# Kernel tuning notes

Hardware: AMD Instinct MI355X
Metric: run time of the kernel (lower is better)

Reference implementation:

```python
import jax, jax.numpy as jnp
import numpy as np

D = 256       # vec_dim
HEADS = 8     # head_num
PS = 4        # patch_size
WS = 7        # window_size (in patches)
P = WS * WS   # tokens per window


def _relative_index():
    # replicates the torch meshgrid / relative coord logic (indexing='ij')
    coords = np.stack(np.meshgrid(np.arange(WS), np.arange(WS), indexing='ij'))  # [2,WS,WS]
    cf = coords.reshape(2, -1)                                                   # [2,P]
    rc = (cf[:, :, None] - cf[:, None, :]).transpose(1, 2, 0)                    # [P,P,2]
    rc[:, :, 0] += WS - 1
    rc[:, :, 1] += WS - 1
    rc[:, :, 1] *= 2 * WS - 1
    return rc.sum(-1)  # [P,P] ints in [0,(2WS-1)^2)


def _shift_mask(ch, cw):
    # standard swin shift mask built on the patch grid (ch, cw)
    fm = np.zeros((ch, cw))
    idx = (slice(0, -WS), slice(-WS, -(WS // 2)), slice(-(WS // 2), None))
    cnt = 0
    for y in idx:
        for x in idx:
            fm[y, x] = cnt
            cnt += 1
    nh, nw = ch // WS, cw // WS
    fm = fm.reshape(nh, WS, nw, WS).transpose(0, 2, 1, 3).reshape(nh * nw, P)
    m = fm[:, None, :] - fm[:, :, None]
    return np.where(m != 0, -100.0, 0.0).astype(np.float32)


def setup_inputs() -> dict:
    key = jax.random.key(0)
    ks = jax.random.split(key, 10)
    N, PN = 8, 3136
    s = 0.02
    return {
        'inputs': jax.random.normal(ks[0], (N, D, PN), jnp.float32),
        'Wk': jax.random.normal(ks[1], (HEADS * D, D), jnp.float32) * s,
        'bk': jax.random.normal(ks[2], (HEADS * D,), jnp.float32) * s,
        'Wq': jax.random.normal(ks[3], (HEADS * D, D), jnp.float32) * s,
        'bq': jax.random.normal(ks[4], (HEADS * D,), jnp.float32) * s,
        'Wv': jax.random.normal(ks[5], (HEADS * D, D), jnp.float32) * s,
        'bv': jax.random.normal(ks[6], (HEADS * D,), jnp.float32) * s,
        'Wo': jax.random.normal(ks[7], (D, HEADS * D), jnp.float32) * s,
        'bo': jax.random.normal(ks[8], (D,), jnp.float32) * s,
        'rel_code': jax.random.normal(ks[9], ((2 * WS - 1) ** 2, HEADS), jnp.float32) * 0.02,
        'h': 224,
        'w': 224,
    }


def _forward(inputs, Wk, bk, Wq, bq, Wv, bv, Wo, bo, rel_code, h, w):
    ch, cw = h // PS, w // PS            # patch grid
    N, _, PN = inputs.shape
    C = D // (PS * PS)
    nh, nw = ch // WS, cw // WS
    WIN = nh * nw

    # patches2features -> pixel-space roll by WS//2 -> features2patches
    x = inputs.reshape(N, C, PS, PS, ch, cw)
    x = x.transpose(0, 1, 4, 2, 5, 3).reshape(N, C, ch * PS, cw * PS)
    x = jnp.roll(x, (WS // 2, WS // 2), axis=(-2, -1))
    x = x.reshape(N, C, ch, PS, cw, PS).transpose(0, 2, 4, 1, 3, 5).reshape(N, PN, D)
    x = x.transpose(0, 2, 1)  # [N,D,PN]

    def proj(W, b):
        e = jnp.einsum('od,ndp->nop', W, x) + b[None, :, None]  # [N,HEADS*D,PN]
        e = e.reshape(N, HEADS, D, ch, cw)
        # window partition: n h d (nh w1)(nw w2) -> n h (nh nw) d (w1 w2)
        e = e.reshape(N, HEADS, D, nh, WS, nw, WS)
        return e.transpose(0, 1, 3, 5, 2, 4, 6).reshape(N, HEADS, WIN, D, P)

    k = proj(Wk, bk)
    q = proj(Wq, bq)
    v = proj(Wv, bv)

    # attn[p,q] = k_p . q_q  (softmax over keys p, axis=3)
    attn = jnp.einsum('nhgdp,nhgdq->nhgpq', k, q) / (D ** 0.5)
    mask = jnp.asarray(_shift_mask(ch, cw))
    attn = attn + mask[None, None]
    rel_idx = _relative_index().ravel()
    rel = rel_code[rel_idx].reshape(P, P, HEADS).transpose(2, 0, 1)  # [H,P,P]
    attn = attn + rel[None, :, None]
    wmap = jax.nn.softmax(attn, axis=3)

    out = jnp.einsum('nhgdp,nhgpq->nhgdq', v, wmap)
    # window merge back to [N,H,D,PN]
    out = out.reshape(N, HEADS, nh, nw, D, WS, WS)
    out = out.transpose(0, 1, 4, 2, 5, 3, 6).reshape(N, HEADS * D, PN)
    return jnp.einsum('od,ndp->nop', Wo, out) + bo[None, :, None]  # [N,D,PN]


def reference(inputs, Wk, bk, Wq, bq, Wv, bv, Wo, bo, rel_code, h, w):
    return _forward(inputs, Wk, bk, Wq, bq, Wv, bv, Wo, bo, rel_code, h, w)
```

## Files before the change

### kernel.cpp

```cpp
#include <hip/hip_runtime.h>
#include <hip/hip_bf16.h>


#define NBATCH 8
#define MSTR   2176
#define TROWS  3200

typedef unsigned short ushort_t;
typedef __attribute__((ext_vector_type(8))) short bf16x8;
typedef __attribute__((ext_vector_type(8))) unsigned short u16x8;
typedef __attribute__((ext_vector_type(4))) float f32x4;

__device__ __forceinline__ float b2f(ushort_t u) {
  union { unsigned int i; float f; } v; v.i = ((unsigned int)u) << 16; return v.f;
}
__device__ __forceinline__ ushort_t f2b(float f) {
  union { float f; unsigned int u; } v; v.f = f;
  unsigned int u = v.u;
  return (ushort_t)((u + 0x7FFFu + ((u >> 16) & 1u)) >> 16);
}
__device__ __forceinline__ int regof(int y) { return (y < 49) ? 0 : ((y < 53) ? 1 : 2); }
__device__ __forceinline__ int div7(int t) { return (t * 37) >> 8; }
__device__ __forceinline__ int tmap(int p, int gi, int gj) {
  int wi = div7(p); return (gi * 7 + wi) * 56 + gj * 7 + (p - wi * 7);
}
__device__ __forceinline__ ushort4 pack4(f32x4 a) {
  ushort4 u; u.x = f2b(a[0]); u.y = f2b(a[1]); u.z = f2b(a[2]); u.w = f2b(a[3]);
  return u;
}
__device__ __forceinline__ void gload_lds16(const ushort_t* g, ushort_t* l) {
  __builtin_amdgcn_global_load_lds(
      (const __attribute__((address_space(1))) void*)g,
      (__attribute__((address_space(3))) void*)l, 16, 0, 0);
}
__device__ __forceinline__ void sb0() { __builtin_amdgcn_sched_barrier(0); }

__global__ void k_prep(const float* __restrict__ Wk, const float* __restrict__ Wq,
                       const float* __restrict__ Wo, const float* __restrict__ Wv,
                       const float* __restrict__ bk, const float* __restrict__ bq,
                       const float* __restrict__ bv, const float* __restrict__ bo,
                       const float* __restrict__ relc,
                       ushort_t* __restrict__ Aext, ushort_t* __restrict__ Wov3,
                       float* __restrict__ cvec, float* __restrict__ relL2) {
  __shared__ float red[8];
  int blk = blockIdx.x, t = threadIdx.x;
  if (blk < 512) {
    int h = blk >> 6, b0 = (blk & 63) << 2, a = t;
    const float* wkh = Wk + h * 65536;
    const float* wqh = Wq + h * 65536;
    float a0 = 0.f, a1 = 0.f, a2 = 0.f, a3 = 0.f;
    for (int dd = 0; dd < 256; ++dd) {
      float wk = wkh[dd * 256 + a];
      float4 w4 = *(const float4*)(wqh + dd * 256 + b0);
      a0 += wk * w4.x; a1 += wk * w4.y; a2 += wk * w4.z; a3 += wk * w4.w;
    }
    ushort4 u; u.x = f2b(a0); u.y = f2b(a1); u.z = f2b(a2); u.w = f2b(a3);
    *(ushort4*)(Aext + (h * 256 + a) * 256 + b0) = u;
  } else if (blk < 1024) {
    int bb = blk - 512;
    int h = bb >> 6, o0 = (bb & 63) << 2, d = t;
    float a0 = 0.f, a1 = 0.f, a2 = 0.f, a3 = 0.f;
    for (int dd = 0; dd < 256; ++dd) {
      float wv = Wv[(h * 256 + dd) * 256 + d];
      a0 += Wo[(o0 + 0) * 2048 + h * 256 + dd] * wv;
      a1 += Wo[(o0 + 1) * 2048 + h * 256 + dd] * wv;
      a2 += Wo[(o0 + 2) * 2048 + h * 256 + dd] * wv;
      a3 += Wo[(o0 + 3) * 2048 + h * 256 + dd] * wv;
    }
    Wov3[(o0 + 0) * 2048 + h * 256 + d] = f2b(a0);
    Wov3[(o0 + 1) * 2048 + h * 256 + d] = f2b(a1);
    Wov3[(o0 + 2) * 2048 + h * 256 + d] = f2b(a2);
    Wov3[(o0 + 3) * 2048 + h * 256 + d] = f2b(a3);
  } else if (blk < 1032) {
    int h = blk - 1024;
    float s1 = 0.f, s2 = 0.f;
    for (int dd = 0; dd < 256; ++dd) {
      s1 += bk[h * 256 + dd] * Wq[(h * 256 + dd) * 256 + t];
      s2 += bq[h * 256 + dd] * Wk[(h * 256 + dd) * 256 + t];
    }
    Aext[(2048 + h) * 256 + t] = f2b(s1);
    Aext[(2056 + h) * 256 + t] = f2b(s2);
  } else if (blk == 1032) {
    for (int i = t; i < 112 * 256 / 8; i += 256)
      *(u16x8*)(Aext + 2064 * 256 + i * 8) = (u16x8){0,0,0,0,0,0,0,0};
  } else if (blk < 1289) {
    int o = blk - 1033;
    const float* wob = Wo + o * 2048;
    float acc = 0.f;
#pragma unroll
    for (int j = 0; j < 8; ++j) acc += wob[j * 256 + t] * bv[j * 256 + t];
#pragma unroll
    for (int s = 1; s < 64; s <<= 1) acc += __shfl_xor(acc, s);
    if ((t & 63) == 0) red[t >> 6] = acc;
    __syncthreads();
    if (t == 0) cvec[o] = bo[o] + red[0] + red[1] + red[2] + red[3];
  } else {
    if (t < 8) {
      float c = 0.f;
      for (int dd = 0; dd < 256; ++dd) c += bk[t * 256 + dd] * bq[t * 256 + dd];
      red[t] = c * 0.0625f;
    }
    __syncthreads();
    for (int i = t; i < 8 * 169; i += 256) {
      int h = i / 169, idx = i - h * 169;
      relL2[i] = relc[idx * 8 + h] + red[h];
    }
  }
}

__global__ void k_conv(const float* __restrict__ X, ushort_t* __restrict__ Xroll) {
  const int n = blockIdx.x / 57, y = blockIdx.x % 57;
  ushort_t* xr = Xroll + (size_t)n * TROWS * 256;
  const int d = threadIdx.x;
  if (y == 56) {
    for (int i = d; i < 64 * 256 / 8; i += 256)
      *(u16x8*)(xr + 3136 * 256 + i * 8) = (u16x8){0,0,0,0,0,0,0,0};
    return;
  }
  const int c = d >> 4, p1 = (d >> 2) & 3, p2 = d & 3;
  const int sp = c * 16 + (((p1 + 1) & 3) << 2) + ((p2 + 1) & 3);
  const int ty = (p1 == 3) ? y : ((y == 0) ? 55 : y - 1);
  const float* rowp = X + (size_t)n * 256 * 3136 + sp * 3136 + ty * 56;
  ushort_t* orow = xr + y * 56 * 256 + d;
  for (int x = 0; x < 56; ++x) {
    int tx = (p2 == 3) ? x : ((x == 0) ? 55 : x - 1);
    orow[x * 256] = f2b(rowp[tx]);
  }
}

__global__ __launch_bounds__(256, 2) void k_gemm1(
    const ushort_t* __restrict__ Xroll, const ushort_t* __restrict__ Aext,
    ushort_t* __restrict__ MT) {
  __shared__ ushort_t Bsm[2][64 * 256];
  const int bx0 = blockIdx.x;
  const int n = bx0 & 7;
  const int inner = bx0 >> 3;
  const int aa = inner % 17;
  const int c  = inner / 17;
  const int a0 = aa * 128;
  const int tstart = (c == 0) ? 0 : (7 * c + 1);
  const int T = (c == 0) ? 8 : 7;
  const int tid = threadIdx.x, wave = tid >> 6, lane = tid & 63;
  const int quad = lane >> 4, l16 = lane & 15;
  const int wa = wave >> 1, wt = wave & 1;
  const ushort_t* Xn = Xroll + (size_t)n * TROWS * 256;
  ushort_t* Mn = MT + (size_t)n * TROWS * MSTR;

  const ushort_t* abase = Aext + (size_t)(a0 + wa * 64 + l16) * 256 + quad * 8;
  bf16x8 areg[8][4];
#pragma unroll
  for (int kk = 0; kk < 8; ++kk)
#pragma unroll
    for (int i = 0; i < 4; ++i)
      areg[kk][i] = *(const bf16x8*)(abase + i * 4096 + kk * 32);
  sb0();

  auto fill = [&](int mt, int b) {
    const ushort_t* src = Xn + (size_t)(tstart + mt) * 64 * 256;
#pragma unroll
    for (int i = 0; i < 8; ++i) {
      int S = i * 256 + tid;
      int rr = S >> 5, sc = S & 31;
      int cc = (sc & 24) | ((sc ^ rr) & 7);
      gload_lds16(src + rr * 256 + cc * 8, &Bsm[b][(i * 256 + wave * 64) * 8]);
    }
  };

  fill(0, 0); sb0();
  fill(1, 1); sb0();
  asm volatile("s_waitcnt vmcnt(8)" ::: "memory"); sb0();
  __builtin_amdgcn_s_barrier(); sb0();

  const int sw = l16 & 7;
  for (int m = 0; m < T; ++m) {
    if (m > 0) {
      if (m + 1 < T) { asm volatile("s_waitcnt vmcnt(16)" ::: "memory"); }
      else           { asm volatile("s_waitcnt vmcnt(8)"  ::: "memory"); }
      sb0();
      __builtin_amdgcn_s_barrier(); sb0();
    }
    const int b = m & 1;
    f32x4 acc[4][2];
#pragma unroll
    for (int i = 0; i < 4; ++i)
#pragma unroll
      for (int j = 0; j < 2; ++j) acc[i][j] = (f32x4){0.f, 0.f, 0.f, 0.f};
#pragma unroll
    for (int kk = 0; kk < 8; ++kk) {
      bf16x8 bfj[2];
#pragma unroll
      for (int j = 0; j < 2; ++j) {
        int rr = wt * 32 + j * 16 + l16;
        int cc = kk * 4 + quad;
        int pos = (cc & 24) | ((cc ^ sw) & 7);
        bfj[j] = *(const bf16x8*)(&Bsm[b][rr * 256 + pos * 8]);
      }
#pragma unroll
      for (int i = 0; i < 4; ++i)
#pragma unroll
        for (int j = 0; j < 2; ++j)
          acc[i][j] = __builtin_amdgcn_mfma_f32_16x16x32_bf16(areg[kk][i], bfj[j], acc[i][j], 0, 0, 0);
    }
    const int tb = (tstart + m) * 64;
#pragma unroll
    for (int i = 0; i < 4; ++i)
#pragma unroll
      for (int j = 0; j < 2; ++j) {
        int tg = tb + wt * 32 + j * 16 + l16;
        int ag = a0 + wa * 64 + i * 16 + quad * 4;
        *(ushort4*)(Mn + (size_t)tg * MSTR + ag) = pack4(acc[i][j]);
      }
    sb0();
    __builtin_amdgcn_s_barrier(); sb0();
    if (m + 2 < T) { fill(m + 2, b); sb0(); }
  }
}

#define XP_STR 264
__global__ __launch_bounds__(512, 4) void k_attn2(
    const ushort_t* __restrict__ Xroll, ushort_t* __restrict__ MT,
    const float* __restrict__ relL2) {
  __shared__ ushort_t Xp[64 * XP_STR];
  __shared__ ushort_t StB[2][64 * 72];
  __shared__ float aqsL[8 * 64];
  __shared__ float bpsL[8 * 64];
  __shared__ float relLh[8 * 169];

  const int tid = threadIdx.x;
  const int wave = tid >> 6, lane = tid & 63;
  const int quad = lane >> 4, l16 = lane & 15;
  const int group = wave >> 2, wv = wave & 3;
  const int n = blockIdx.x >> 6, g = blockIdx.x & 63;
  const int gi = g >> 3, gj = g & 7;
  const ushort_t* Xn = Xroll + (size_t)n * TROWS * 256;
  ushort_t* Mn = MT + (size_t)n * TROWS * MSTR;

  {
    const int p = tid & 63, cg = tid >> 6;
    if (p < 49) {
      int t = tmap(p, gi, gj);
#pragma unroll
      for (int i = 0; i < 4; ++i)
        *(u16x8*)(&Xp[p * XP_STR + (cg * 4 + i) * 8]) =
            *(const u16x8*)(Xn + t * 256 + (cg * 4 + i) * 8);
    } else {
#pragma unroll
      for (int i = 0; i < 4; ++i)
        *(u16x8*)(&Xp[p * XP_STR + (cg * 4 + i) * 8]) = (u16x8){0,0,0,0,0,0,0,0};
    }
  }
  for (int i = tid; i < 8 * 169; i += 512) relLh[i] = relL2[i];
  {
    const int h = tid >> 6, q = tid & 63;
    int qq = (q < 49) ? q : 48;
    int t = tmap(qq, gi, gj);
    aqsL[h * 64 + q] = b2f(Mn[(size_t)t * MSTR + 2048 + h]);
    bpsL[h * 64 + q] = b2f(Mn[(size_t)t * MSTR + 2056 + h]);
  }
  __syncthreads();

  bf16x8 xfr[4][2];
#pragma unroll
  for (int dt = 0; dt < 4; ++dt) {
    const int d = (wv * 4 + dt) * 16 + l16;
#pragma unroll
    for (int kk = 0; kk < 2; ++kk)
#pragma unroll
      for (int j = 0; j < 8; ++j)
        xfr[dt][kk][j] = (short)Xp[(kk * 32 + quad * 8 + j) * XP_STR + d];
  }

  const int q = wv * 16 + l16;
  const int qq = (q < 49) ? q : 48;
  const int tq = tmap(qq, gi, gj);
  const ushort_t* Mbase = Mn + (size_t)tq * MSTR + quad * 8;
  const int yq = div7(qq), xq = qq - yq * 7;
  const int fq = regof(gi * 7 + yq) * 3 + regof(gj * 7 + xq);

  for (int hh = 0; hh < 4; ++hh) {
    const int h = hh * 2 + group;
    f32x4 sacc[4];
#pragma unroll
    for (int pt = 0; pt < 4; ++pt) sacc[pt] = (f32x4){0.f, 0.f, 0.f, 0.f};
    const ushort_t* mrow = Mbase + h * 256;
#pragma unroll
    for (int kk = 0; kk < 8; ++kk) {
      bf16x8 bfm = *(const bf16x8*)(mrow + kk * 32);
#pragma unroll
      for (int pt = 0; pt < 4; ++pt) {
        bf16x8 af = *(const bf16x8*)(&Xp[(pt * 16 + l16) * XP_STR + kk * 32 + quad * 8]);
        sacc[pt] = __builtin_amdgcn_mfma_f32_16x16x32_bf16(af, bfm, sacc[pt], 0, 0, 0);
      }
    }
    float v[16];
    const float aqv = aqsL[h * 64 + q];
    const float* rel_h = &relLh[h * 169];
    float m = -1e30f;
#pragma unroll
    for (int pt = 0; pt < 4; ++pt)
#pragma unroll
      for (int r = 0; r < 4; ++r) {
        int p = pt * 16 + quad * 4 + r;
        float val = -1e30f;
        if (p < 49) {
          int yp = div7(p), xp = p - yp * 7;
          int fp = regof(gi * 7 + yp) * 3 + regof(gj * 7 + xp);
          val = (sacc[pt][r] + aqv + bpsL[h * 64 + p]) * 0.0625f +
                rel_h[(yp - yq + 6) + 13 * (xp - xq + 6)];
          if (fp != fq) val -= 100.f;
        }
        v[pt * 4 + r] = val;
        m = fmaxf(m, val);
      }
    m = fmaxf(m, __shfl_xor(m, 16));
    m = fmaxf(m, __shfl_xor(m, 32));
    float s = 0.f;
#pragma unroll
    for (int i = 0; i < 16; ++i) { v[i] = __expf(v[i] - m); s += v[i]; }
    s += __shfl_xor(s, 16);
    s += __shfl_xor(s, 32);
    const float inv = 1.f / s;
    __syncthreads();
    {
      ushort_t* sb = &StB[group][q * 72];
#pragma unroll
      for (int pt = 0; pt < 4; ++pt) {
        ushort4 u;
        u.x = f2b(v[pt * 4 + 0] * inv); u.y = f2b(v[pt * 4 + 1] * inv);
        u.z = f2b(v[pt * 4 + 2] * inv); u.w = f2b(v[pt * 4 + 3] * inv);
        *(ushort4*)(&sb[pt * 16 + quad * 4]) = u;
      }
    }
    __syncthreads();
#pragma unroll
    for (int qt = 0; qt < 4; ++qt) {
      f32x4 tacc[4];
#pragma unroll
      for (int dt = 0; dt < 4; ++dt) tacc[dt] = (f32x4){0.f, 0.f, 0.f, 0.f};
#pragma unroll
      for (int kk = 0; kk < 2; ++kk) {
        bf16x8 bfw = *(const bf16x8*)(&StB[group][(qt * 16 + l16) * 72 + kk * 32 + quad * 8]);
#pragma unroll
        for (int dt = 0; dt < 4; ++dt)
          tacc[dt] = __builtin_amdgcn_mfma_f32_16x16x32_bf16(xfr[dt][kk], bfw, tacc[dt], 0, 0, 0);
      }
      int q2 = qt * 16 + l16;
      if (q2 < 49) {
        int t2 = tmap(q2, gi, gj);
#pragma unroll
        for (int dt = 0; dt < 4; ++dt) {
          int d0 = (wv * 4 + dt) * 16 + quad * 4;
          *(ushort4*)(Mn + (size_t)t2 * MSTR + h * 256 + d0) = pack4(tacc[dt]);
        }
      }
    }
  }
}

__global__ __launch_bounds__(256, 2) void k_gemm3(
    const ushort_t* __restrict__ Wov3, const ushort_t* __restrict__ MT,
    const float* __restrict__ cvec, float* __restrict__ out) {
  __shared__ ushort_t Asm[128 * 128];
  __shared__ ushort_t Bsm[128 * 128];
  const int bx0 = blockIdx.x;
  const int bx = (bx0 & 7) * 50 + (bx0 >> 3);
  const int n = bx / 50, r2 = bx % 50;
  const int oi = r2 / 25, tt = r2 % 25;
  const int o0 = oi * 128, t0 = tt * 128;
  const int tid = threadIdx.x, wave = tid >> 6, lane = tid & 63;
  const int quad = lane >> 4, l16 = lane & 15;
  const int wa = wave >> 1, wt = wave & 1;
  const ushort_t* Tn = MT + (size_t)n * TROWS * MSTR;
  float* on = out + (size_t)n * 256 * 3136;
  const int sw = l16 & 7;

  f32x4 acc[4][4];
#pragma unroll
  for (int i = 0; i < 4; ++i)
#pragma unroll
    for (int j = 0; j < 4; ++j) acc[i][j] = (f32x4){0.f, 0.f, 0.f, 0.f};

  for (int kit = 0; kit < 16; ++kit) {
    const int kb = kit * 128;
#pragma unroll
    for (int i = 0; i < 8; ++i) {
      int S = i * 256 + tid;
      int rr = S >> 4, sc = S & 15;
      int c = (sc & 8) | ((sc ^ rr) & 7);
      gload_lds16(Wov3 + (o0 + rr) * 2048 + kb + c * 8,
                  &Asm[(i * 256 + wave * 64) * 8]);
    }
#pragma unroll
    for (int i = 0; i < 8; ++i) {
      int S = i * 256 + tid;
      int rr = S >> 4, sc = S & 15;
      int c = (sc & 8) | ((sc ^ rr) & 7);
      gload_lds16(Tn + (size_t)(t0 + rr) * MSTR + kb + c * 8,
                  &Bsm[(i * 256 + wave * 64) * 8]);
    }
    __syncthreads();
#pragma unroll
    for (int kk = 0; kk < 4; ++kk) {
      bf16x8 af[4], bf[4];
      const int c = kk * 4 + quad;
      const int pos = (c & 8) | ((c ^ sw) & 7);
#pragma unroll
      for (int i = 0; i < 4; ++i)
        af[i] = *(const bf16x8*)(&Asm[(wa * 64 + i * 16 + l16) * 128 + pos * 8]);
#pragma unroll
      for (int j = 0; j < 4; ++j)
        bf[j] = *(const bf16x8*)(&Bsm[(wt * 64 + j * 16 + l16) * 128 + pos * 8]);
#pragma unroll
      for (int i = 0; i < 4; ++i)
#pragma unroll
        for (int j = 0; j < 4; ++j)
          acc[i][j] = __builtin_amdgcn_mfma_f32_16x16x32_bf16(af[i], bf[j], acc[i][j], 0, 0, 0);
    }
    __syncthreads();
  }
#pragma unroll
  for (int i = 0; i < 4; ++i) {
    const int ob = o0 + wa * 64 + i * 16 + quad * 4;
    const float4 cv = *(const float4*)(cvec + ob);
#pragma unroll
    for (int j = 0; j < 4; ++j) {
      const int tg = t0 + wt * 64 + j * 16 + l16;
      if (tg < 3136) {
        on[(size_t)(ob + 0) * 3136 + tg] = acc[i][j][0] + cv.x;
        on[(size_t)(ob + 1) * 3136 + tg] = acc[i][j][1] + cv.y;
        on[(size_t)(ob + 2) * 3136 + tg] = acc[i][j][2] + cv.z;
        on[(size_t)(ob + 3) * 3136 + tg] = acc[i][j][3] + cv.w;
      }
    }
  }
}

extern "C" void kernel_launch(void* const* d_in, const int* in_sizes, int n_in,
                              void* d_out, int out_size, void* d_ws, size_t ws_size,
                              hipStream_t stream) {
  (void)in_sizes; (void)n_in; (void)out_size; (void)ws_size;
  const float* X  = (const float*)d_in[0];
  const float* Wk = (const float*)d_in[1];
  const float* bk = (const float*)d_in[2];
  const float* Wq = (const float*)d_in[3];
  const float* bq = (const float*)d_in[4];
  const float* Wv = (const float*)d_in[5];
  const float* bv = (const float*)d_in[6];
  const float* Wo = (const float*)d_in[7];
  const float* bo = (const float*)d_in[8];
  const float* rc = (const float*)d_in[9];

  ushort_t* MT    = (ushort_t*)d_ws;
  ushort_t* Xroll = MT + (size_t)8 * TROWS * MSTR;
  ushort_t* Aext  = Xroll + (size_t)8 * TROWS * 256;
  ushort_t* Wov3  = Aext + 2176 * 256;
  float* fbase = (float*)(Wov3 + 256 * 2048);
  float* cvec  = fbase;
  float* relL2 = fbase + 256;
  float* out = (float*)d_out;

  k_prep <<<dim3(1290), dim3(256), 0, stream>>>(Wk, Wq, Wo, Wv, bk, bq, bv, bo, rc,
                                                Aext, Wov3, cvec, relL2);
  k_conv <<<dim3(8 * 57), dim3(256), 0, stream>>>(X, Xroll);
  k_gemm1<<<dim3(8 * 119), dim3(256), 0, stream>>>(Xroll, Aext, MT);
  k_attn2<<<dim3(8 * 64), dim3(512), 0, stream>>>(Xroll, MT, relL2);
  k_gemm3<<<dim3(8 * 50), dim3(256), 0, stream>>>(Wov3, MT, cvec, out);
}
```

Baseline: 274.2 us.

## Load GEMM1 B operand directly from global into registers, dropping LDS double buffer

The first projection GEMM no longer stages X tiles through a double-buffered shared-memory buffer filled by async global-to-LDS loads. Each wave now loads its B fragments straight from global memory into registers every iteration, which removes the LDS footprint and all block barriers. In exchange, waves that share a tile each read it separately through cache rather than sharing one LDS copy. Loads are also no longer prefetched ahead of the MFMA work, so memory latency may be exposed.

```diff
diff --git a/kernel.cpp b/kernel.cpp
--- a/kernel.cpp
+++ b/kernel.cpp
@@ -131,7 +131,6 @@
 __global__ __launch_bounds__(256, 2) void k_gemm1(
     const ushort_t* __restrict__ Xroll, const ushort_t* __restrict__ Aext,
     ushort_t* __restrict__ MT) {
-  __shared__ ushort_t Bsm[2][64 * 256];
   const int bx0 = blockIdx.x;
   const int n = bx0 & 7;
   const int inner = bx0 >> 3;
@@ -155,52 +154,32 @@
       areg[kk][i] = *(const bf16x8*)(abase + i * 4096 + kk * 32);
   sb0();
 
-  auto fill = [&](int mt, int b) {
-    const ushort_t* src = Xn + (size_t)(tstart + mt) * 64 * 256;
-#pragma unroll
-    for (int i = 0; i < 8; ++i) {
-      int S = i * 256 + tid;
-      int rr = S >> 5, sc = S & 31;
-      int cc = (sc & 24) | ((sc ^ rr) & 7);
-      gload_lds16(src + rr * 256 + cc * 8, &Bsm[b][(i * 256 + wave * 64) * 8]);
-    }
-  };
-
-  fill(0, 0); sb0();
-  fill(1, 1); sb0();
-  asm volatile("s_waitcnt vmcnt(8)" ::: "memory"); sb0();
-  __builtin_amdgcn_s_barrier(); sb0();
-
-  const int sw = l16 & 7;
+  const ushort_t* bbase =
+      Xn + (size_t)(tstart * 64 + wt * 32 + l16) * 256 + quad * 8;
+
   for (int m = 0; m < T; ++m) {
-    if (m > 0) {
-      if (m + 1 < T) { asm volatile("s_waitcnt vmcnt(16)" ::: "memory"); }
-      else           { asm volatile("s_waitcnt vmcnt(8)"  ::: "memory"); }
-      sb0();
-      __builtin_amdgcn_s_barrier(); sb0();
-    }
-    const int b = m & 1;
+    const ushort_t* bsrc = bbase + (size_t)m * 64 * 256;
+    bf16x8 breg[8][2];
+#pragma unroll
+    for (int kk = 0; kk < 8; ++kk)
+#pragma unroll
+      for (int j = 0; j < 2; ++j)
+        breg[kk][j] = *(const bf16x8*)(bsrc + j * 16 * 256 + kk * 32);
+    sb0();
+
     f32x4 acc[4][2];
 #pragma unroll
     for (int i = 0; i < 4; ++i)
 #pragma unroll
       for (int j = 0; j < 2; ++j) acc[i][j] = (f32x4){0.f, 0.f, 0.f, 0.f};
 #pragma unroll
-    for (int kk = 0; kk < 8; ++kk) {
-      bf16x8 bfj[2];
-#pragma unroll
-      for (int j = 0; j < 2; ++j) {
-        int rr = wt * 32 + j * 16 + l16;
-        int cc = kk * 4 + quad;
-        int pos = (cc & 24) | ((cc ^ sw) & 7);
-        bfj[j] = *(const bf16x8*)(&Bsm[b][rr * 256 + pos * 8]);
-      }
+    for (int kk = 0; kk < 8; ++kk)
 #pragma unroll
       for (int i = 0; i < 4; ++i)
 #pragma unroll
         for (int j = 0; j < 2; ++j)
-          acc[i][j] = __builtin_amdgcn_mfma_f32_16x16x32_bf16(areg[kk][i], bfj[j], acc[i][j], 0, 0, 0);
-    }
+          acc[i][j] = __builtin_amdgcn_mfma_f32_16x16x32_bf16(areg[kk][i], breg[kk][j], acc[i][j], 0, 0, 0);
+
     const int tb = (tstart + m) * 64;
 #pragma unroll
     for (int i = 0; i < 4; ++i)
@@ -210,9 +189,6 @@
         int ag = a0 + wa * 64 + i * 16 + quad * 4;
         *(ushort4*)(Mn + (size_t)tg * MSTR + ag) = pack4(acc[i][j]);
       }
-    sb0();
-    __builtin_amdgcn_s_barrier(); sb0();
-    if (m + 2 < T) { fill(m + 2, b); sb0(); }
   }
 }
 
```

New measurement: 311.5 us. +13.6%, slower.
